# Performance work log

Measured on AMD Instinct MI355X. Metric: run time of the kernel, lower is better.

## Reference

```python
import jax, jax.numpy as jnp
import numpy as np
import math

B, S, D, H, DFF = 16, 1024, 512, 8, 2048
DH = D // H
EPS = 1e-5


def setup_inputs() -> dict:
    key = jax.random.key(0)
    ks = jax.random.split(key, 16)
    sc = 0.02
    inp = {
        "x": jax.random.normal(ks[0], (B, S, D), dtype=jnp.float32),
        "mask": jnp.zeros((B, 1, 1, S), dtype=jnp.float32),
        # attention projections (stored as [in, out])
        "wq": jax.random.normal(ks[1], (D, D), jnp.float32) * sc,
        "bq": jnp.zeros((D,), jnp.float32),
        "wk": jax.random.normal(ks[2], (D, D), jnp.float32) * sc,
        "bk": jnp.zeros((D,), jnp.float32),
        "wv": jax.random.normal(ks[3], (D, D), jnp.float32) * sc,
        "bv": jnp.zeros((D,), jnp.float32),
        "wo": jax.random.normal(ks[4], (D, D), jnp.float32) * sc,
        "bo": jnp.zeros((D,), jnp.float32),
        # FFN
        "w1": jax.random.normal(ks[5], (D, DFF), jnp.float32) * sc,
        "b1": jnp.zeros((DFF,), jnp.float32),
        "w2": jax.random.normal(ks[6], (DFF, D), jnp.float32) * sc,
        "b2": jnp.zeros((D,), jnp.float32),
        # LayerNorms over the full [S, D] slab (normalized_shape=[S, D])
        "ln1_w": jnp.ones((S, D), jnp.float32),
        "ln1_b": jnp.zeros((S, D), jnp.float32),
        "ln2_w": jnp.ones((S, D), jnp.float32),
        "ln2_b": jnp.zeros((S, D), jnp.float32),
    }
    return inp


def _layernorm_2d(x, w, b):
    # torch nn.LayerNorm([S, D]): normalize jointly over last two dims
    m = jnp.mean(x, axis=(-2, -1), keepdims=True)
    v = jnp.mean(jnp.square(x - m), axis=(-2, -1), keepdims=True)
    return (x - m) * jax.lax.rsqrt(v + EPS) * w + b


def _encoder_layer(x, mask, wq, bq, wk, bk, wv, bv, wo, bo,
                   w1, b1, w2, b2, ln1_w, ln1_b, ln2_w, ln2_b):
    # --- multi-head attention ---
    def heads(t):  # [B,S,D] -> [B,H,S,DH]
        return t.reshape(B, S, H, DH).transpose(0, 2, 1, 3)

    q = heads(x @ wq + bq)
    k = heads(x @ wk + bk)
    v = heads(x @ wv + bv)

    logits = jnp.einsum("bhqd,bhkd->bhqk", q, k) / math.sqrt(DH)
    logits = logits + mask * -1e9
    attn = jax.nn.softmax(logits, axis=-1)          # [B,H,S,S]
    ctx = jnp.einsum("bhqk,bhkd->bhqd", attn, v)    # [B,H,S,DH]
    ctx = ctx.transpose(0, 2, 1, 3).reshape(B, S, D)
    attn_out = ctx @ wo + bo

    out1 = _layernorm_2d(x + attn_out, ln1_w, ln1_b)

    # --- FFN ---
    ffn = jax.nn.relu(out1 @ w1 + b1) @ w2 + b2
    out2 = _layernorm_2d(out1 + ffn, ln2_w, ln2_b)
    return out2


def reference(x, mask, wq, bq, wk, bk, wv, bv, wo, bo,
              w1, b1, w2, b2, ln1_w, ln1_b, ln2_w, ln2_b):
    return _encoder_layer(x, mask, wq, bq, wk, bk, wv, bv, wo, bo,
                          w1, b1, w2, b2, ln1_w, ln1_b, ln2_w, ln2_b)
```

## Files before the change

kernel.cpp:

```cpp
#include <hip/hip_runtime.h>
#include <stdint.h>

#define B_   16
#define S_   1024
#define D_   512
#define H_   8
#define DH_  64
#define DFF_ 2048
#define M_   (B_*S_)
#define SD_  (S_*D_)
#define NT_  16

typedef unsigned short u16;
typedef unsigned int u32;
typedef __attribute__((ext_vector_type(2))) unsigned int u32x2;
typedef __attribute__((ext_vector_type(4))) unsigned short u16x4;
typedef __attribute__((ext_vector_type(8))) short bf16x8;
typedef __attribute__((ext_vector_type(4))) float f32x4;
typedef __attribute__((ext_vector_type(16))) float f32x16;

#define LOG2E 1.4426950408889634f

#if defined(__has_builtin)
#if __has_builtin(__builtin_amdgcn_permlane32_swap)
#define HAVE_PLS 1
#endif
#endif

__device__ __forceinline__ u16 f2bf(float f) {
  union { float f; uint32_t u; } x{f};
  uint32_t r = x.u + 0x7fffu + ((x.u >> 16) & 1u);
  return (u16)(r >> 16);
}

__device__ __forceinline__ float bf2f(u16 v) {
  union { uint32_t u; float f; } x{(uint32_t)v << 16};
  return x.f;
}

__device__ __forceinline__ u32 pk2(float lo, float hi) {
  union { float f; u32 u; } a{lo}, b{hi};
  return __builtin_amdgcn_perm(b.u, a.u, 0x07060302u);
}

__device__ __forceinline__ float exp2fast(float x) {
#if __has_builtin(__builtin_amdgcn_exp2f)
  return __builtin_amdgcn_exp2f(x);
#else
  return exp2f(x);
#endif
}

__device__ __forceinline__ void gload16(const u16* g, u16* l) {
  __builtin_amdgcn_global_load_lds(
      (const __attribute__((address_space(1))) uint32_t*)g,
      (__attribute__((address_space(3))) uint32_t*)l, 16, 0, 0);
}

__device__ __forceinline__ int swz3(int r) { return (r & 7) ^ ((r >> 3) & 7); }

__global__ __launch_bounds__(256) void prep_kernel(
    const float* __restrict__ x, u16* __restrict__ xb,
    const float* __restrict__ wq, const float* __restrict__ wk,
    const float* __restrict__ wv, const float* __restrict__ wo,
    const float* __restrict__ w1, const float* __restrict__ w2,
    u16* __restrict__ wqkvT, u16* __restrict__ woT,
    u16* __restrict__ w1T, u16* __restrict__ w2T) {
  int bid = blockIdx.x, tid = threadIdx.x;
  if (bid < 8192) {
    int i = bid * 256 + tid;
    f32x4 v = ((const f32x4*)x)[i];
    u16x4 o = { f2bf(v[0]), f2bf(v[1]), f2bf(v[2]), f2bf(v[3]) };
    ((u16x4*)xb)[i] = o;
    return;
  }
  bid -= 8192;
  const float* W; u16* WT; int K, N, bx, by;
  if (bid < 1024) {
    int which = bid >> 8;
    W  = (which == 0) ? wq : (which == 1) ? wk : (which == 2) ? wv : wo;
    WT = (which == 3) ? woT : (wqkvT + (size_t)which * 512 * 512);
    K = 512; N = 512;
    int r = bid & 255; bx = r & 15; by = r >> 4;
  } else if (bid < 2048) {
    int r = bid - 1024; W = w1; WT = w1T; K = 512; N = 2048;
    bx = r & 63; by = r >> 6;
  } else {
    int r = bid - 2048; W = w2; WT = w2T; K = 2048; N = 512;
    bx = r & 15; by = r >> 4;
  }
  __shared__ float t[32][33];
  int n0 = bx * 32, k0 = by * 32;
  int tx = tid & 31, ty = tid >> 5;
  #pragma unroll
  for (int i = 0; i < 4; i++)
    t[ty + 8*i][tx] = W[(size_t)(k0 + ty + 8*i) * N + n0 + tx];
  __syncthreads();
  #pragma unroll
  for (int i = 0; i < 4; i++)
    WT[(size_t)(n0 + ty + 8*i) * K + k0 + tx] = f2bf(t[tx][ty + 8*i]);
}

__global__ __launch_bounds__(256) void gemm128_bk64_kernel(
    const u16* __restrict__ A, const u16* __restrict__ WT,
    const float* __restrict__ bias0, const u16* __restrict__ resB,
    u16* __restrict__ out0,
    float* __restrict__ partOut, int K, int N, int nx, int ypg) {
  __shared__ u16 lA[2][128 * 64];
  __shared__ u16 lB[2][128 * 64];
  __shared__ float lred[8];
  int tid = threadIdx.x;
  int lane = tid & 63, wid = tid >> 6;
  int wr = wid >> 1, wc = wid & 1;
  int lrow = lane & 15, kg = lane >> 4;

  int dd = blockIdx.x;
  int cc = dd & 7, jj = dd >> 3;
  int bx = jj % nx, by = cc * ypg + jj / nx;
  int m0 = by * 128, n0 = bx * 128;

  int r0 = tid >> 3;
  int c0s = ((tid & 7) ^ (r0 & 7)) * 8;
  const u16* agp = A  + (size_t)m0 * K;
  const u16* bgp = WT + (size_t)n0 * K;

  int aoff[4], boff[4];
  #pragma unroll
  for (int mi = 0; mi < 4; mi++) {
    int row = wr*64 + mi*16 + lrow;
    aoff[mi] = row*64 + ((kg ^ (row & 7)) * 8);
  }
  #pragma unroll
  for (int ni = 0; ni < 4; ni++) {
    int row = wc*64 + ni*16 + lrow;
    boff[ni] = row*64 + ((kg ^ (row & 7)) * 8);
  }

  f32x4 z = {0.f, 0.f, 0.f, 0.f};
  f32x4 acc[4][4];
  #pragma unroll
  for (int mi = 0; mi < 4; mi++)
    #pragma unroll
    for (int ni = 0; ni < 4; ni++) acc[mi][ni] = z;

#define STG64(buf, kt) do { \
    _Pragma("unroll") \
    for (int j = 0; j < 4; j++) { \
      gload16(agp + (size_t)(r0 + j*32) * K + (kt) + c0s, &lA[buf][(tid + j*256) * 8]); \
      gload16(bgp + (size_t)(r0 + j*32) * K + (kt) + c0s, &lB[buf][(tid + j*256) * 8]); \
    } \
  } while (0)

  STG64(0, 0);

  int nk = K / 64;
  int cur = 0;
  for (int t = 0; t < nk; t++) {
    __syncthreads();
    if (t + 1 < nk) STG64(cur ^ 1, (t + 1) * 64);
    #pragma unroll
    for (int kk = 0; kk < 2; kk++) {
      int xr = kk ? 32 : 0;
      bf16x8 af[4], bfv[4];
      #pragma unroll
      for (int mi = 0; mi < 4; mi++)
        af[mi] = *(const bf16x8*)&lA[cur][aoff[mi] ^ xr];
      #pragma unroll
      for (int ni = 0; ni < 4; ni++)
        bfv[ni] = *(const bf16x8*)&lB[cur][boff[ni] ^ xr];
      __builtin_amdgcn_s_setprio(1);
      #pragma unroll
      for (int mi = 0; mi < 4; mi++)
        #pragma unroll
        for (int ni = 0; ni < 4; ni++)
          acc[mi][ni] = __builtin_amdgcn_mfma_f32_16x16x32_bf16(af[mi], bfv[ni], acc[mi][ni], 0, 0, 0);
      __builtin_amdgcn_s_setprio(0);
    }
    cur ^= 1;
  }
#undef STG64

  float s_acc = 0.f, q_acc = 0.f;
  #pragma unroll
  for (int mi = 0; mi < 4; mi++)
    #pragma unroll
    for (int ni = 0; ni < 4; ni++) {
      int col = n0 + wc*64 + ni*16 + lrow;
      float bv = bias0[col];
      #pragma unroll
      for (int r = 0; r < 4; r++) {
        int row = m0 + wr*64 + mi*16 + kg*4 + r;
        size_t off = (size_t)row * N + col;
        float tv = acc[mi][ni][r] + bv + bf2f(resB[off]);
        out0[off] = f2bf(tv);
        s_acc += tv;
        q_acc += tv * tv;
      }
    }

  #pragma unroll
  for (int dsh = 1; dsh < 64; dsh <<= 1) {
    s_acc += __shfl_xor(s_acc, dsh);
    q_acc += __shfl_xor(q_acc, dsh);
  }
  if (lane == 0) { lred[wid*2] = s_acc; lred[wid*2+1] = q_acc; }
  __syncthreads();
  if (tid == 0) {
    int batch = by >> 3;
    int pidx = batch*32 + (by & 7)*nx + bx;
    partOut[pidx*2]   = lred[0]+lred[2]+lred[4]+lred[6];
    partOut[pidx*2+1] = lred[1]+lred[3]+lred[5]+lred[7];
  }
}

__global__ __launch_bounds__(256) void gemm128_bk64_qkv_kernel(
    const u16* __restrict__ A, const u16* __restrict__ WT,
    const float* __restrict__ bq, const float* __restrict__ bk,
    const float* __restrict__ bv,
    u16* __restrict__ Qb, u16* __restrict__ Kb, u16* __restrict__ Vb,
    int K, int nx, int ypg) {
  __shared__ u16 lA[2][128 * 64];
  __shared__ u16 lB[2][128 * 64];
  int tid = threadIdx.x;
  int lane = tid & 63, wid = tid >> 6;
  int wr = wid >> 1, wc = wid & 1;
  int lrow = lane & 15, kg = lane >> 4;

  int dd = blockIdx.x;
  int cc = dd & 7, jj = dd >> 3;
  int bx = jj % nx, by = cc * ypg + jj / nx;
  int m0 = by * 128, n0 = bx * 128;

  int r0 = tid >> 3;
  int c0s = ((tid & 7) ^ (r0 & 7)) * 8;
  const u16* agp = A  + (size_t)m0 * K;
  const u16* bgp = WT + (size_t)n0 * K;

  int aoff[4], boff[4];
  #pragma unroll
  for (int mi = 0; mi < 4; mi++) {
    int row = wr*64 + mi*16 + lrow;
    aoff[mi] = row*64 + ((kg ^ (row & 7)) * 8);
  }
  #pragma unroll
  for (int ni = 0; ni < 4; ni++) {
    int row = wc*64 + ni*16 + lrow;
    boff[ni] = row*64 + ((kg ^ (row & 7)) * 8);
  }

  f32x4 z = {0.f, 0.f, 0.f, 0.f};
  f32x4 acc[4][4];
  #pragma unroll
  for (int mi = 0; mi < 4; mi++)
    #pragma unroll
    for (int ni = 0; ni < 4; ni++) acc[mi][ni] = z;

#define STG64(buf, kt) do { \
    _Pragma("unroll") \
    for (int j = 0; j < 4; j++) { \
      gload16(agp + (size_t)(r0 + j*32) * K + (kt) + c0s, &lA[buf][(tid + j*256) * 8]); \
      gload16(bgp + (size_t)(r0 + j*32) * K + (kt) + c0s, &lB[buf][(tid + j*256) * 8]); \
    } \
  } while (0)

  STG64(0, 0);

  int nk = K / 64;
  int cur = 0;
  for (int t = 0; t < nk; t++) {
    __syncthreads();
    if (t + 1 < nk) STG64(cur ^ 1, (t + 1) * 64);
    #pragma unroll
    for (int kk = 0; kk < 2; kk++) {
      int xr = kk ? 32 : 0;
      bf16x8 af[4], bfv[4];
      #pragma unroll
      for (int mi = 0; mi < 4; mi++)
        af[mi] = *(const bf16x8*)&lA[cur][aoff[mi] ^ xr];
      #pragma unroll
      for (int ni = 0; ni < 4; ni++)
        bfv[ni] = *(const bf16x8*)&lB[cur][boff[ni] ^ xr];
      __builtin_amdgcn_s_setprio(1);
      #pragma unroll
      for (int mi = 0; mi < 4; mi++)
        #pragma unroll
        for (int ni = 0; ni < 4; ni++)
          acc[mi][ni] = __builtin_amdgcn_mfma_f32_16x16x32_bf16(af[mi], bfv[ni], acc[mi][ni], 0, 0, 0);
      __builtin_amdgcn_s_setprio(0);
    }
    cur ^= 1;
  }
#undef STG64

  int seg = n0 >> 9;
  const float* bp = (seg == 0) ? bq : (seg == 1) ? bk : bv;
  u16* op = (seg == 0) ? Qb : (seg == 1) ? Kb : Vb;
  float aeff = (seg == 0) ? 0.125f * LOG2E : 1.0f;

  #pragma unroll
  for (int mi = 0; mi < 4; mi++)
    #pragma unroll
    for (int ni = 0; ni < 4; ni++) {
      int col = n0 + wc*64 + ni*16 + lrow;
      int ocol = col & 511;
      float bvv = bp[ocol];
      #pragma unroll
      for (int r = 0; r < 4; r++) {
        int row = m0 + wr*64 + mi*16 + kg*4 + r;
        float v = (acc[mi][ni][r] + bvv) * aeff;
        op[(size_t)row * 512 + ocol] = f2bf(v);
      }
    }
}

template<bool RELU>
__global__ __launch_bounds__(512, 4) void gemm128x256_kernel(
    const u16* __restrict__ A, const u16* __restrict__ WT,
    const float* __restrict__ bias0,
    u16* __restrict__ out0, int K, int N, int nx, int ypg) {
  __shared__ u16 lA[2][128 * 32];
  __shared__ u16 lB[2][256 * 32];
  int tid = threadIdx.x;
  int lane = tid & 63, wid = tid >> 6;
  int wr = wid >> 2, wc = wid & 3;
  int lrow = lane & 15, kg = lane >> 4;

  int dd = blockIdx.x;
  int cc = dd & 7, jj = dd >> 3;
  int bx = jj % nx, by = cc * ypg + jj / nx;
  int m0 = by * 128, n0 = bx * 256;

  int r0 = tid >> 2;
  int c0s = ((tid & 3) ^ ((r0 >> 1) & 3)) * 8;
  const u16* agp = A  + (size_t)m0 * K;
  const u16* bgp = WT + (size_t)n0 * K;

  int aoff[4], boff[4];
  #pragma unroll
  for (int mi = 0; mi < 4; mi++) {
    int row = wr*64 + mi*16 + lrow;
    aoff[mi] = row*32 + ((kg ^ ((row >> 1) & 3)) * 8);
  }
  #pragma unroll
  for (int ni = 0; ni < 4; ni++) {
    int row = wc*64 + ni*16 + lrow;
    boff[ni] = row*32 + ((kg ^ ((row >> 1) & 3)) * 8);
  }

  f32x4 z = {0.f, 0.f, 0.f, 0.f};
  f32x4 acc[4][4];
  #pragma unroll
  for (int mi = 0; mi < 4; mi++)
    #pragma unroll
    for (int ni = 0; ni < 4; ni++) acc[mi][ni] = z;

#define STG(buf, kt) do { \
    gload16(agp + (size_t)r0 * K + (kt) + c0s,         &lA[buf][tid * 8]); \
    gload16(bgp + (size_t)r0 * K + (kt) + c0s,         &lB[buf][tid * 8]); \
    gload16(bgp + (size_t)(r0 + 128) * K + (kt) + c0s, &lB[buf][4096 + tid * 8]); \
  } while (0)

  STG(0, 0);

  int nk = K / 32;
  int cur = 0;
  for (int t = 0; t < nk; t++) {
    __syncthreads();
    if (t + 1 < nk) STG(cur ^ 1, (t + 1) * 32);
    bf16x8 af[4], bfv[4];
    #pragma unroll
    for (int mi = 0; mi < 4; mi++)
      af[mi] = *(const bf16x8*)&lA[cur][aoff[mi]];
    #pragma unroll
    for (int ni = 0; ni < 4; ni++)
      bfv[ni] = *(const bf16x8*)&lB[cur][boff[ni]];
    __builtin_amdgcn_s_setprio(1);
    #pragma unroll
    for (int mi = 0; mi < 4; mi++)
      #pragma unroll
      for (int ni = 0; ni < 4; ni++)
        acc[mi][ni] = __builtin_amdgcn_mfma_f32_16x16x32_bf16(af[mi], bfv[ni], acc[mi][ni], 0, 0, 0);
    __builtin_amdgcn_s_setprio(0);
    cur ^= 1;
  }
#undef STG

  #pragma unroll
  for (int mi = 0; mi < 4; mi++)
    #pragma unroll
    for (int ni = 0; ni < 4; ni++) {
      int col = n0 + wc*64 + ni*16 + lrow;
      float bv = bias0[col];
      #pragma unroll
      for (int r = 0; r < 4; r++) {
        int row = m0 + wr*64 + mi*16 + kg*4 + r;
        float v = acc[mi][ni][r] + bv;
        if (RELU) v = fmaxf(v, 0.f);
        out0[(size_t)row * N + col] = f2bf(v);
      }
    }
}

__global__ __launch_bounds__(512) void attn_kernel(
    const u16* __restrict__ Q, const u16* __restrict__ Km,
    const u16* __restrict__ Vm, const float* __restrict__ mask,
    u16* __restrict__ ctx) {
  __shared__ u16 lK[2][4096];
  __shared__ u16 lV[2][4096];
  __shared__ float lBias[1024];
  int tid = threadIdx.x, lane = tid & 63, wid = tid >> 6;
  int la = lane & 31, hi = lane >> 5;
  int wg = blockIdx.x;
  int xcd = wg & 7, idx = wg >> 3;
  int bh = xcd * 16 + (idx & 15);
  int qt = idx >> 4;
  int b = bh >> 3, h = bh & 7;
  bool vwave = (wid < 4);
  int tid2 = tid & 255;

  const u16* qp = Q + (size_t)(b*S_ + qt*256 + wid*32 + la) * D_ + h*DH_ + hi*8;
  bf16x8 qf[4];
  #pragma unroll
  for (int c = 0; c < 4; c++) qf[c] = *(const bf16x8*)(qp + c*16);

  int krow = tid2 >> 3;
  int kcol = 8 * (tid2 & 7);
  int kc0 = kcol ^ (swz3(krow) << 3);
  int kc1 = kcol ^ (swz3(krow + 32) << 3);
  int va = tid & 7, vp = (tid >> 3) & 31;
  const u16* kbase = Km + ((size_t)b*S_) * D_ + h*DH_;
  const u16* vbase = Vm + ((size_t)b*S_) * D_ + h*DH_ + 8*va;

#define STAGE_K(buf, tt) do { \
    const u16* kt_ = kbase + (size_t)(tt)*64*D_; \
    gload16(kt_ + (size_t)krow*D_ + kc0,        &lK[buf][tid2*8]); \
    gload16(kt_ + (size_t)(krow+32)*D_ + kc1,   &lK[buf][2048 + tid2*8]); \
  } while (0)
#define LOAD_V(tt) do { \
    const u16* vt_ = vbase + (size_t)((tt)*64 + 2*vp) * D_; \
    nv0 = *(const bf16x8*)vt_; nv1 = *(const bf16x8*)(vt_ + D_); \
  } while (0)
#define WRITE_V(buf) do { \
    u32* lVd_ = (u32*)lV[buf]; \
    _Pragma("unroll") \
    for (int jv = 0; jv < 8; jv++) { \
      int row_ = 8*va + jv; \
      u32 pv_ = (u32)(u16)nv0[jv] | ((u32)(u16)nv1[jv] << 16); \
      lVd_[row_*32 + (vp ^ (swz3(row_) << 2))] = pv_; \
    } \
  } while (0)

  int swk0 = swz3(la) << 2, swk1 = swz3(la + 32) << 2;
  f32x16 oc0, oc1;
  #pragma unroll
  for (int i = 0; i < 16; i++) { oc0[i] = 0.f; oc1[i] = 0.f; }
  float lsum = 0.f;

#define QKT(d0, d1, tt) do { \
    _Pragma("unroll") \
    for (int rq = 0; rq < 4; rq++) { \
      f32x4 bb0 = *(const f32x4*)&lBias[(tt)*64 + rq*8 + hi*4]; \
      f32x4 bb1 = *(const f32x4*)&lBias[(tt)*64 + 32 + rq*8 + hi*4]; \
      _Pragma("unroll") \
      for (int jj = 0; jj < 4; jj++) { d0[rq*4+jj] = bb0[jj]; d1[rq*4+jj] = bb1[jj]; } \
    } \
    { const u16* lkb_ = lK[(tt)&1]; \
      __builtin_amdgcn_s_setprio(1); \
      _Pragma("unroll") \
      for (int c_ = 0; c_ < 4; c_++) { \
        int dwb_ = c_*8 + hi*4; \
        bf16x8 kf0_ = *(const bf16x8*)&lkb_[la*64 + ((dwb_ ^ swk0) << 1)]; \
        bf16x8 kf1_ = *(const bf16x8*)&lkb_[(la+32)*64 + ((dwb_ ^ swk1) << 1)]; \
        d0 = __builtin_amdgcn_mfma_f32_32x32x16_bf16(kf0_, qf[c_], d0, 0, 0, 0); \
        d1 = __builtin_amdgcn_mfma_f32_32x32x16_bf16(kf1_, qf[c_], d1, 0, 0, 0); \
      } \
      __builtin_amdgcn_s_setprio(0); } \
  } while (0)

#define SOFTPV(s0v, s1v, tt) do { \
    float rsp_[4] = {0.f, 0.f, 0.f, 0.f}; \
    _Pragma("unroll") \
    for (int i_ = 0; i_ < 16; i_++) { float e_ = exp2fast(s0v[i_]); s0v[i_] = e_; rsp_[i_ & 3] += e_; } \
    _Pragma("unroll") \
    for (int i_ = 0; i_ < 16; i_++) { float e_ = exp2fast(s1v[i_]); s1v[i_] = e_; rsp_[i_ & 3] += e_; } \
    lsum += (rsp_[0] + rsp_[1]) + (rsp_[2] + rsp_[3]); \
    { const u16* lvb_ = lV[(tt)&1]; \
      __builtin_amdgcn_s_setprio(1); \
      _Pragma("unroll") \
      for (int cc_ = 0; cc_ < 4; cc_++) { \
        const int base_ = 8 * (cc_ & 1); \
        float pv_[8]; \
        _Pragma("unroll") \
        for (int k_ = 0; k_ < 8; k_++) pv_[k_] = (cc_ < 2) ? s0v[base_ + k_] : s1v[base_ + k_]; \
        u32 a0_ = pk2(pv_[0], pv_[1]); \
        u32 a1_ = pk2(pv_[2], pv_[3]); \
        u32 b0_ = pk2(pv_[4], pv_[5]); \
        u32 b1_ = pk2(pv_[6], pv_[7]); \
        union { u32 u[4]; bf16x8 v; } pf_; \
        PEXCH(pf_, a0_, a1_, b0_, b1_); \
        _Pragma("unroll") \
        for (int vb_ = 0; vb_ < 2; vb_++) { \
          int row_ = vb_*32 + la; \
          int dwv_ = (cc_*8 + hi*4) ^ (swz3(row_) << 2); \
          bf16x8 vf_ = *(const bf16x8*)&lvb_[row_*64 + (dwv_ << 1)]; \
          if (vb_ == 0) oc0 = __builtin_amdgcn_mfma_f32_32x32x16_bf16(pf_.v, vf_, oc0, 0, 0, 0); \
          else          oc1 = __builtin_amdgcn_mfma_f32_32x32x16_bf16(pf_.v, vf_, oc1, 0, 0, 0); \
        } \
      } \
      __builtin_amdgcn_s_setprio(0); } \
  } while (0)

#ifdef HAVE_PLS
#define PEXCH(pf_, a0_, a1_, b0_, b1_) do { \
    u32x2 r0_ = __builtin_amdgcn_permlane32_swap(a0_, b0_, false, false); \
    u32x2 r1_ = __builtin_amdgcn_permlane32_swap(a1_, b1_, false, false); \
    pf_.u[0] = r0_[0]; pf_.u[1] = r1_[0]; pf_.u[2] = r0_[1]; pf_.u[3] = r1_[1]; \
  } while (0)
#else
#define PEXCH(pf_, a0_, a1_, b0_, b1_) do { \
    u32 sd0_ = hi ? a0_ : b0_, sd1_ = hi ? a1_ : b1_; \
    u32 x0_ = (u32)__shfl_xor((int)sd0_, 32); \
    u32 x1_ = (u32)__shfl_xor((int)sd1_, 32); \
    pf_.u[0] = hi ? x0_ : a0_; \
    pf_.u[1] = hi ? x1_ : a1_; \
    pf_.u[2] = hi ? b0_ : x0_; \
    pf_.u[3] = hi ? b1_ : x1_; \
  } while (0)
#endif

  bf16x8 nv0, nv1;
  if (vwave) {
    f32x4 mv = ((const f32x4*)(mask + (size_t)b*S_))[tid];
    f32x4 bv;
    #pragma unroll
    for (int jj = 0; jj < 4; jj++) bv[jj] = mv[jj] * (-1.0e9f * LOG2E);
    ((f32x4*)lBias)[tid] = bv;
    LOAD_V(0);
    WRITE_V(0);
    LOAD_V(1);
  } else {
    STAGE_K(0, 0);
    STAGE_K(1, 1);
  }
  __syncthreads();

  f32x16 sA0, sA1, sB0, sB1;
  QKT(sA0, sA1, 0);
  __syncthreads();

  for (int t = 0; t < NT_; t += 2) {
    if (!vwave) { if (t + 2 < NT_) STAGE_K(t & 1, t + 2); }
    if (vwave) {
      WRITE_V((t + 1) & 1);
      if (t + 2 < NT_) LOAD_V(t + 2);
    }
    QKT(sB0, sB1, t + 1);
    SOFTPV(sA0, sA1, t);
    __syncthreads();
    {
      int u = t + 1;
      if (!vwave) { if (u + 2 < NT_) STAGE_K(u & 1, u + 2); }
      if (vwave) {
        if (u + 1 < NT_) WRITE_V((u + 1) & 1);
        if (u + 2 < NT_) LOAD_V(u + 2);
      }
      if (u + 1 < NT_) QKT(sA0, sA1, u + 1);
      SOFTPV(sB0, sB1, u);
      __syncthreads();
    }
  }
#undef STAGE_K
#undef LOAD_V
#undef WRITE_V
#undef QKT
#undef SOFTPV
#undef PEXCH

  lsum += __shfl_xor(lsum, 32);
  float linv = 1.f / lsum;
  #pragma unroll
  for (int r = 0; r < 16; r++) {
    int qr = (r&3) + 8*(r>>2) + 4*hi;
    float lr = __shfl(linv, qr);
    size_t rowoff = (size_t)(b*S_ + qt*256 + wid*32 + qr) * D_ + h*DH_;
    ctx[rowoff + la]      = f2bf(oc0[r] * lr);
    ctx[rowoff + 32 + la] = f2bf(oc1[r] * lr);
  }
}

template<bool WB, bool WF>
__global__ __launch_bounds__(256) void ln_apply_kernel(
    const u16* __restrict__ r, const float* __restrict__ part,
    const float* __restrict__ w, const float* __restrict__ bb,
    float* __restrict__ outF, u16* __restrict__ outB) {
  int b = blockIdx.y, c = blockIdx.x, tid = threadIdx.x;
  float s = 0.f, q = 0.f;
  for (int i = 0; i < 32; i++) { s += part[(b*32+i)*2]; q += part[(b*32+i)*2+1]; }
  const float inv = 1.f / (float)SD_;
  float mean = s * inv;
  float var = q * inv - mean * mean;
  float rs = rsqrtf(var + 1e-5f);
  size_t base = (size_t)b * SD_;
  #pragma unroll
  for (int i = 0; i < 8; i++) {
    int li4 = c*2048 + i*256 + tid;
    u16x4 rv = ((const u16x4*)(r + base))[li4];
    f32x4 wv = ((const f32x4*)w)[li4];
    f32x4 bv = ((const f32x4*)bb)[li4];
    f32x4 ov;
    #pragma unroll
    for (int jj = 0; jj < 4; jj++) ov[jj] = (bf2f(rv[jj]) - mean) * rs * wv[jj] + bv[jj];
    if (WF) ((f32x4*)(outF + base))[li4] = ov;
    if (WB) {
      u16x4 ub = { f2bf(ov[0]), f2bf(ov[1]), f2bf(ov[2]), f2bf(ov[3]) };
      ((u16x4*)(outB + base))[li4] = ub;
    }
  }
}

extern "C" void kernel_launch(void* const* d_in, const int* in_sizes, int n_in,
                              void* d_out, int out_size, void* d_ws, size_t ws_size,
                              hipStream_t stream) {
  (void)in_sizes; (void)n_in; (void)out_size; (void)ws_size;
  const float* x    = (const float*)d_in[0];
  const float* mask = (const float*)d_in[1];
  const float* wq = (const float*)d_in[2];
  const float* bq = (const float*)d_in[3];
  const float* wk = (const float*)d_in[4];
  const float* bk = (const float*)d_in[5];
  const float* wv = (const float*)d_in[6];
  const float* bv = (const float*)d_in[7];
  const float* wo = (const float*)d_in[8];
  const float* bo = (const float*)d_in[9];
  const float* w1 = (const float*)d_in[10];
  const float* b1 = (const float*)d_in[11];
  const float* w2 = (const float*)d_in[12];
  const float* b2 = (const float*)d_in[13];
  const float* ln1w = (const float*)d_in[14];
  const float* ln1b = (const float*)d_in[15];
  const float* ln2w = (const float*)d_in[16];
  const float* ln2b = (const float*)d_in[17];
  float* out = (float*)d_out;

  char* ws = (char*)d_ws;
  const size_t MB = 1ull << 20;
  u16*   xb    = (u16*)(ws + 0);
  u16*   Qb    = (u16*)(ws + 16*MB);
  u16*   Kb    = (u16*)(ws + 32*MB);
  u16*   Vb    = (u16*)(ws + 48*MB);
  u16*   ctxb  = (u16*)(ws + 64*MB);
  u16*   res1b = (u16*)(ws + 80*MB);
  u16*   out1b = (u16*)(ws + 0);
  u16*   ffn1  = (u16*)(ws + 16*MB);
  u16*   res2b = (u16*)(ws + 112*MB);
  float* part  = (float*)(ws + 144*MB);
  u16*   wqkvT = (u16*)(ws + 145*MB);
  u16*   woT   = (u16*)(ws + 147*MB);
  u16*   w1T   = (u16*)(ws + 148*MB);
  u16*   w2T   = (u16*)(ws + 150*MB);

  prep_kernel<<<11264, 256, 0, stream>>>(
      x, xb, wq, wk, wv, wo, w1, w2, wqkvT, woT, w1T, w2T);

  gemm128_bk64_qkv_kernel<<<1536, 256, 0, stream>>>(
      xb, wqkvT, bq, bk, bv, Qb, Kb, Vb, 512, 12, 16);

  attn_kernel<<<512, 512, 0, stream>>>(Qb, Kb, Vb, mask, ctxb);

  gemm128_bk64_kernel<<<512, 256, 0, stream>>>(
      ctxb, woT, bo, xb, res1b, part, 512, 512, 4, 16);

  ln_apply_kernel<true,false><<<dim3(64,16), 256, 0, stream>>>(
      res1b, part, ln1w, ln1b, nullptr, out1b);

  gemm128x256_kernel<true><<<1024, 512, 0, stream>>>(
      out1b, w1T, b1, ffn1, 512, 2048, 8, 16);

  gemm128_bk64_kernel<<<512, 256, 0, stream>>>(
      ffn1, w2T, b2, out1b, res2b, part, 2048, 512, 4, 16);

  ln_apply_kernel<false,true><<<dim3(64,16), 256, 0, stream>>>(
      res2b, part, ln2w, ln2b, out, nullptr);
}
```

Before: 214.9 us.

## Process 128-key tiles per barrier in attention to halve syncs

The attention loop now stages 128 keys of K and V per LDS buffer instead of 64, so each iteration handles two 64-key halves and there are 8 iterations instead of 16. This halves the number of block-wide barriers and simplifies the software pipeline to a single-stage prefetch. In exchange LDS use doubles to about 68 KB, which may reduce occupancy. It also drops the interleaving in which the next tile's QK^T overlapped the current softmax·V, so MFMA and exp work are less overlapped.

```diff
diff --git a/kernel.cpp b/kernel.cpp
--- a/kernel.cpp
+++ b/kernel.cpp
@@ -9,7 +9,7 @@
 #define DFF_ 2048
 #define M_   (B_*S_)
 #define SD_  (S_*D_)
-#define NT_  16
+#define NT2_ 8
 
 typedef unsigned short u16;
 typedef unsigned int u32;
@@ -405,8 +405,8 @@
     const u16* __restrict__ Q, const u16* __restrict__ Km,
     const u16* __restrict__ Vm, const float* __restrict__ mask,
     u16* __restrict__ ctx) {
-  __shared__ u16 lK[2][4096];
-  __shared__ u16 lV[2][4096];
+  __shared__ u16 lK[2][8192];
+  __shared__ u16 lV[2][8192];
   __shared__ float lBias[1024];
   int tid = threadIdx.x, lane = tid & 63, wid = tid >> 6;
   int la = lane & 31, hi = lane >> 5;
@@ -432,21 +432,26 @@
   const u16* vbase = Vm + ((size_t)b*S_) * D_ + h*DH_ + 8*va;
 
 #define STAGE_K(buf, tt) do { \
-    const u16* kt_ = kbase + (size_t)(tt)*64*D_; \
+    const u16* kt_ = kbase + (size_t)(tt)*128*D_; \
     gload16(kt_ + (size_t)krow*D_ + kc0,        &lK[buf][tid2*8]); \
     gload16(kt_ + (size_t)(krow+32)*D_ + kc1,   &lK[buf][2048 + tid2*8]); \
+    gload16(kt_ + (size_t)(krow+64)*D_ + kc0,   &lK[buf][4096 + tid2*8]); \
+    gload16(kt_ + (size_t)(krow+96)*D_ + kc1,   &lK[buf][6144 + tid2*8]); \
   } while (0)
 #define LOAD_V(tt) do { \
-    const u16* vt_ = vbase + (size_t)((tt)*64 + 2*vp) * D_; \
+    const u16* vt_ = vbase + (size_t)((tt)*128 + 2*vp) * D_; \
     nv0 = *(const bf16x8*)vt_; nv1 = *(const bf16x8*)(vt_ + D_); \
+    const u16* vu_ = vbase + (size_t)((tt)*128 + 64 + 2*vp) * D_; \
+    nv2 = *(const bf16x8*)vu_; nv3 = *(const bf16x8*)(vu_ + D_); \
   } while (0)
 #define WRITE_V(buf) do { \
     u32* lVd_ = (u32*)lV[buf]; \
     _Pragma("unroll") \
     for (int jv = 0; jv < 8; jv++) { \
       int row_ = 8*va + jv; \
-      u32 pv_ = (u32)(u16)nv0[jv] | ((u32)(u16)nv1[jv] << 16); \
-      lVd_[row_*32 + (vp ^ (swz3(row_) << 2))] = pv_; \
+      int cs_ = vp ^ (swz3(row_) << 2); \
+      lVd_[row_*64 + cs_]      = (u32)(u16)nv0[jv] | ((u32)(u16)nv1[jv] << 16); \
+      lVd_[row_*64 + 32 + cs_] = (u32)(u16)nv2[jv] | ((u32)(u16)nv3[jv] << 16); \
     } \
   } while (0)
 
@@ -456,15 +461,15 @@
   for (int i = 0; i < 16; i++) { oc0[i] = 0.f; oc1[i] = 0.f; }
   float lsum = 0.f;
 
-#define QKT(d0, d1, tt) do { \
+#define QKT(d0, d1, tt, hh) do { \
     _Pragma("unroll") \
     for (int rq = 0; rq < 4; rq++) { \
-      f32x4 bb0 = *(const f32x4*)&lBias[(tt)*64 + rq*8 + hi*4]; \
-      f32x4 bb1 = *(const f32x4*)&lBias[(tt)*64 + 32 + rq*8 + hi*4]; \
+      f32x4 bb0 = *(const f32x4*)&lBias[(tt)*128 + (hh)*64 + rq*8 + hi*4]; \
+      f32x4 bb1 = *(const f32x4*)&lBias[(tt)*128 + (hh)*64 + 32 + rq*8 + hi*4]; \
       _Pragma("unroll") \
       for (int jj = 0; jj < 4; jj++) { d0[rq*4+jj] = bb0[jj]; d1[rq*4+jj] = bb1[jj]; } \
     } \
-    { const u16* lkb_ = lK[(tt)&1]; \
+    { const u16* lkb_ = &lK[(tt)&1][(hh)*4096]; \
       __builtin_amdgcn_s_setprio(1); \
       _Pragma("unroll") \
       for (int c_ = 0; c_ < 4; c_++) { \
@@ -477,7 +482,7 @@
       __builtin_amdgcn_s_setprio(0); } \
   } while (0)
 
-#define SOFTPV(s0v, s1v, tt) do { \
+#define SOFTPV(s0v, s1v, tt, hh) do { \
     float rsp_[4] = {0.f, 0.f, 0.f, 0.f}; \
     _Pragma("unroll") \
     for (int i_ = 0; i_ < 16; i_++) { float e_ = exp2fast(s0v[i_]); s0v[i_] = e_; rsp_[i_ & 3] += e_; } \
@@ -502,7 +507,7 @@
         for (int vb_ = 0; vb_ < 2; vb_++) { \
           int row_ = vb_*32 + la; \
           int dwv_ = (cc_*8 + hi*4) ^ (swz3(row_) << 2); \
-          bf16x8 vf_ = *(const bf16x8*)&lvb_[row_*64 + (dwv_ << 1)]; \
+          bf16x8 vf_ = *(const bf16x8*)&lvb_[row_*128 + (((hh)*32 + dwv_) << 1)]; \
           if (vb_ == 0) oc0 = __builtin_amdgcn_mfma_f32_32x32x16_bf16(pf_.v, vf_, oc0, 0, 0, 0); \
           else          oc1 = __builtin_amdgcn_mfma_f32_32x32x16_bf16(pf_.v, vf_, oc1, 0, 0, 0); \
         } \
@@ -528,7 +533,7 @@
   } while (0)
 #endif
 
-  bf16x8 nv0, nv1;
+  bf16x8 nv0, nv1, nv2, nv3;
   if (vwave) {
     f32x4 mv = ((const f32x4*)(mask + (size_t)b*S_))[tid];
     f32x4 bv;
@@ -537,37 +542,23 @@
     ((f32x4*)lBias)[tid] = bv;
     LOAD_V(0);
     WRITE_V(0);
-    LOAD_V(1);
   } else {
     STAGE_K(0, 0);
-    STAGE_K(1, 1);
   }
   __syncthreads();
 
   f32x16 sA0, sA1, sB0, sB1;
-  QKT(sA0, sA1, 0);
-  __syncthreads();
-
-  for (int t = 0; t < NT_; t += 2) {
-    if (!vwave) { if (t + 2 < NT_) STAGE_K(t & 1, t + 2); }
-    if (vwave) {
-      WRITE_V((t + 1) & 1);
-      if (t + 2 < NT_) LOAD_V(t + 2);
+  for (int t = 0; t < NT2_; t++) {
+    if (t + 1 < NT2_) {
+      if (!vwave) STAGE_K((t + 1) & 1, t + 1);
+      if (vwave)  LOAD_V(t + 1);
     }
-    QKT(sB0, sB1, t + 1);
-    SOFTPV(sA0, sA1, t);
+    QKT(sA0, sA1, t, 0);
+    QKT(sB0, sB1, t, 1);
+    SOFTPV(sA0, sA1, t, 0);
+    SOFTPV(sB0, sB1, t, 1);
+    if (t + 1 < NT2_ && vwave) WRITE_V((t + 1) & 1);
     __syncthreads();
-    {
-      int u = t + 1;
-      if (!vwave) { if (u + 2 < NT_) STAGE_K(u & 1, u + 2); }
-      if (vwave) {
-        if (u + 1 < NT_) WRITE_V((u + 1) & 1);
-        if (u + 2 < NT_) LOAD_V(u + 2);
-      }
-      if (u + 1 < NT_) QKT(sA0, sA1, u + 1);
-      SOFTPV(sB0, sB1, u);
-      __syncthreads();
-    }
   }
 #undef STAGE_K
 #undef LOAD_V
```

Measured after the change: 215.7 us. No clear change (+0.4%).
